# Optimization experiments

Measured on AMD Instinct MI355X. Metric: run time of the kernel, lower is better.

Reference implementation:

```python
import jax, jax.numpy as jnp
import numpy as np

B, N, HID = 4, 1024, 256
NH, DH = 8, 32          # heads, head dim (HID = NH*DH)
BH = 64                 # bias MLP hidden


def setup_inputs() -> dict:
    key = jax.random.key(0)
    ks = jax.random.split(key, 12)
    s = lambda fan_in: 1.0 / np.sqrt(fan_in)
    return {
        "h": jax.random.normal(ks[0], (B, N, HID), jnp.float32),
        "coord": jax.random.uniform(ks[1], (B, N), jnp.float32),
        "mask": jnp.ones((B, N), jnp.int32),
        # qkv / proj linear params (stored [in, out])
        "Wqkv": jax.random.normal(ks[2], (HID, 3 * HID), jnp.float32) * s(HID),
        "bqkv": jnp.zeros((3 * HID,), jnp.float32),
        "Wproj": jax.random.normal(ks[3], (HID, HID), jnp.float32) * s(HID),
        "bproj": jnp.zeros((HID,), jnp.float32),
        # layernorm
        "gamma": jnp.ones((HID,), jnp.float32),
        "beta": jnp.zeros((HID,), jnp.float32),
        # relative-bias MLP: Linear(1->BH), SiLU, Linear(BH->BH), SiLU, Linear(BH->NH)
        "Wb1": jax.random.normal(ks[4], (1, BH), jnp.float32),
        "bb1": jnp.zeros((BH,), jnp.float32),
        "Wb2": jax.random.normal(ks[5], (BH, BH), jnp.float32) * s(BH),
        "bb2": jnp.zeros((BH,), jnp.float32),
        "Wb3": jax.random.normal(ks[6], (BH, NH), jnp.float32) * s(BH),
        "bb3": jnp.zeros((NH,), jnp.float32),
    }


def _layernorm(x, gamma, beta, eps=1e-5):
    mu = jnp.mean(x, axis=-1, keepdims=True)
    var = jnp.mean((x - mu) ** 2, axis=-1, keepdims=True)
    return (x - mu) * jax.lax.rsqrt(var + eps) * gamma + beta


def reference(h, coord, mask, Wqkv, bqkv, Wproj, bproj, gamma, beta,
              Wb1, bb1, Wb2, bb2, Wb3, bb3):
    x = _layernorm(h, gamma, beta)                      # [B,N,HID]
    qkv = x @ Wqkv + bqkv                               # [B,N,3*HID]
    q, k, v = jnp.split(qkv, 3, axis=-1)
    # [B,N,HID] -> [B,NH,N,DH]
    reshape = lambda t: t.reshape(B, N, NH, DH).transpose(0, 2, 1, 3)
    q, k, v = reshape(q), reshape(k), reshape(v)

    attn = jnp.einsum("bhqd,bhkd->bhqk", q, k) / np.sqrt(DH).astype(np.float32)

    # pairwise coordinate differences and learned bias
    dcoord = coord[:, None, :] - coord[:, :, None]      # [B,N,N]
    t = dcoord[..., None]                               # [B,N,N,1]
    t = jax.nn.silu(t @ Wb1 + bb1)                      # [B,N,N,BH]
    t = jax.nn.silu(t @ Wb2 + bb2)                      # [B,N,N,BH]
    bias = (t @ Wb3 + bb3)                              # [B,N,N,NH]
    attn = attn + bias.transpose(0, 3, 1, 2)            # [B,NH,N,N]

    neg_inf = jnp.array(-jnp.inf, attn.dtype)
    attn = jnp.where(mask[:, None, None, :] == 0, neg_inf, attn)
    w = jax.nn.softmax(attn, axis=-1)

    out = jnp.einsum("bhqk,bhkd->bhqd", w, v)           # [B,NH,N,DH]
    out = out.transpose(0, 2, 1, 3).reshape(B, N, HID)
    out = out @ Wproj + bproj
    return h + out
```

## Files before the change

### kernel.cpp

```cpp
#include <hip/hip_runtime.h>
#include <hip/hip_fp16.h>
#include <hip/hip_bf16.h>
#include <math.h>

#define BB   4
#define NN   1024
#define HIDD 256
#define NHD  8
#define DHD  32
#define BHD  64
#define TI2  2048
#define TBSX 3592
#define NSPL 2
#define LOG2E 1.4426950408889634f

typedef __attribute__((ext_vector_type(8))) short bf16x8;
typedef __attribute__((ext_vector_type(4))) short bf16x4;
typedef __attribute__((ext_vector_type(4))) float f32x4;

__device__ __forceinline__ unsigned short f2bf(float x) {
  union { __hip_bfloat16 h; unsigned short u; } c;
  c.h = __float2bfloat16(x);
  return c.u;
}
__device__ __forceinline__ float bf2f(unsigned short b) {
  union { unsigned u; float f; } c; c.u = ((unsigned)b) << 16;
  return c.f;
}

__device__ __forceinline__ void pv_mfma(f32x4& acc, bf16x4 a, bf16x4 b) {
#if __has_builtin(__builtin_amdgcn_mfma_f32_16x16x16bf16_1k)
  acc = __builtin_amdgcn_mfma_f32_16x16x16bf16_1k(a, b, acc, 0, 0, 0);
#else
  asm volatile("s_nop 1\n\t"
               "v_mfma_f32_16x16x16_bf16 %0, %1, %2, %0\n\t"
               "s_nop 7\n\t"
               "s_nop 3"
               : "+v"(acc) : "v"(a), "v"(b));
#endif
}

__global__ __launch_bounds__(256) void prep_kernel(
    const float* __restrict__ Wb1, const float* __restrict__ bb1,
    const float* __restrict__ Wb2, const float* __restrict__ bb2,
    const float* __restrict__ Wb3, const float* __restrict__ bb3,
    const float* __restrict__ Wqkv, const float* __restrict__ Wproj,
    unsigned short* __restrict__ tblb, unsigned short* __restrict__ wtq,
    unsigned short* __restrict__ wtp)
{
  __shared__ float h1a[4][64], h2a[4][64];
  __shared__ float t[16][17];
  int bid = blockIdx.x, tid = threadIdx.x;
  if (bid < 513) {
    int g = tid >> 6, j = tid & 63;
    int pt = bid * 4 + g;
    float tt = -1.0f + (float)pt * (2.0f / (float)TI2);
    float z0 = fmaf(tt, Wb1[j], bb1[j]);
    h1a[g][j] = z0 / (1.0f + __expf(-z0));
    __syncthreads();
    float a0 = bb2[j];
    #pragma unroll 16
    for (int i = 0; i < BHD; ++i) a0 = fmaf(h1a[g][i], Wb2[i*BHD + j], a0);
    h2a[g][j] = a0 / (1.0f + __expf(-a0));
    __syncthreads();
    if (j < NHD && pt <= TI2) {
      float o0 = bb3[j];
      #pragma unroll 16
      for (int i = 0; i < BHD; ++i) o0 = fmaf(h2a[g][i], Wb3[i*NHD + j], o0);
      tblb[j*TBSX + pt] = f2bf(o0 * LOG2E);
    }
  } else if (bid < 521) {
    int head = bid - 513;
    unsigned short neg = f2bf(-1e31f);
    for (int i = tid; i < TBSX - (TI2 + 1); i += 256)
      tblb[head*TBSX + TI2 + 1 + i] = neg;
  } else {
    const float* W; unsigned short* Wt; int n0, k0, ncols;
    if (bid < 1289) {
      int rb = bid - 521;
      n0 = (rb % 48) * 16; k0 = (rb / 48) * 16; ncols = 768;
      W = Wqkv; Wt = wtq;
    } else {
      int rc = bid - 1289;
      n0 = (rc & 15) * 16; k0 = (rc >> 4) * 16; ncols = 256;
      W = Wproj; Wt = wtp;
    }
    int sx = tid & 15, sy = tid >> 4;
    t[sy][sx] = W[(size_t)(k0 + sy) * ncols + n0 + sx];
    __syncthreads();
    Wt[(size_t)(n0 + sy) * 256 + k0 + sx] = f2bf(t[sx][sy]);
  }
}

__global__ __launch_bounds__(256) void ln_qkv_mm_kernel(
    const float* __restrict__ h, const float* __restrict__ gamma,
    const float* __restrict__ beta, const unsigned short* __restrict__ Wt,
    const float* __restrict__ bqkv,
    unsigned short* __restrict__ qws, unsigned short* __restrict__ kws,
    unsigned short* __restrict__ vtws)
{
  __shared__ unsigned short xs[16][260];
  int tid = threadIdx.x;
  int m0 = blockIdx.x * 16, n0 = blockIdx.y * 128;

  {
    int r = tid >> 4, q = tid & 15;
    const float* hrow = h + (size_t)(m0 + r)*HIDD + q*16;
    float4 xv[4];
    float sum = 0.f, sq = 0.f;
    #pragma unroll
    for (int j = 0; j < 4; ++j) {
      xv[j] = *(const float4*)&hrow[j*4];
      sum += xv[j].x + xv[j].y + xv[j].z + xv[j].w;
      sq  += xv[j].x*xv[j].x + xv[j].y*xv[j].y + xv[j].z*xv[j].z + xv[j].w*xv[j].w;
    }
    sum += __shfl_xor(sum, 1); sq += __shfl_xor(sq, 1);
    sum += __shfl_xor(sum, 2); sq += __shfl_xor(sq, 2);
    sum += __shfl_xor(sum, 4); sq += __shfl_xor(sq, 4);
    sum += __shfl_xor(sum, 8); sq += __shfl_xor(sq, 8);
    float mu  = sum * (1.0f/HIDD);
    float var = sq  * (1.0f/HIDD) - mu*mu;
    float rs  = rsqrtf(var + 1e-5f);
    #pragma unroll
    for (int j2 = 0; j2 < 2; ++j2) {
      union { bf16x8 v; unsigned short u[8]; } o;
      #pragma unroll
      for (int e = 0; e < 2; ++e) {
        float4 x4 = xv[j2*2 + e];
        int col = q*16 + j2*8 + e*4;
        float4 gv = *(const float4*)&gamma[col];
        float4 bv = *(const float4*)&beta[col];
        o.u[e*4+0] = f2bf(fmaf((x4.x - mu)*rs, gv.x, bv.x));
        o.u[e*4+1] = f2bf(fmaf((x4.y - mu)*rs, gv.y, bv.y));
        o.u[e*4+2] = f2bf(fmaf((x4.z - mu)*rs, gv.z, bv.z));
        o.u[e*4+3] = f2bf(fmaf((x4.w - mu)*rs, gv.w, bv.w));
      }
      *(bf16x8*)&xs[r][q*16 + j2*8] = o.v;
    }
  }
  __syncthreads();

  int lane = tid & 63, w = tid >> 6;
  int lo = lane & 15, hi = lane >> 4;
  int cw = w * 32;
  f32x4 acc[2];
  acc[0] = (f32x4){0.f,0.f,0.f,0.f};
  acc[1] = (f32x4){0.f,0.f,0.f,0.f};

  #pragma unroll
  for (int ks = 0; ks < 8; ++ks) {
    bf16x8 af = *(const bf16x8*)&xs[lo][ks*32 + hi*8];
    #pragma unroll
    for (int nt = 0; nt < 2; ++nt) {
      bf16x8 bf = *(const bf16x8*)&Wt[(size_t)(n0 + cw + nt*16 + lo)*256 + ks*32 + hi*8];
      acc[nt] = __builtin_amdgcn_mfma_f32_16x16x32_bf16(af, bf, acc[nt], 0, 0, 0);
    }
  }

  int b = m0 >> 10;
  if (n0 < 512) {
    unsigned short* dst = (n0 < 256) ? qws : kws;
    int nbase = (m0 & 1023) + hi*4;
    #pragma unroll
    for (int nt = 0; nt < 2; ++nt) {
      int c = n0 + cw + nt*16 + lo;
      int cr = c & 255;
      int head = cr >> 5, d = cr & 31;
      float bq = bqkv[c];
      size_t bh = (size_t)(b*NHD + head);
      #pragma unroll
      for (int r = 0; r < 4; ++r)
        dst[(bh*NN + nbase + r)*DHD + d] = f2bf(acc[nt][r] + bq);
    }
  } else {
    __syncthreads();
    unsigned short (*vt)[20] = (unsigned short(*)[20])&xs[0][0];
    #pragma unroll
    for (int nt = 0; nt < 2; ++nt) {
      int cr = cw + nt*16 + lo;
      float bq = bqkv[n0 + cr];
      union { unsigned short u[4]; unsigned wd[2]; } pk;
      #pragma unroll
      for (int r = 0; r < 4; ++r) pk.u[r] = f2bf(acc[nt][r] + bq);
      int col = hi*4;
      *(unsigned*)&vt[cr][col]     = pk.wd[0];
      *(unsigned*)&vt[cr][col + 2] = pk.wd[1];
    }
    __syncthreads();
    int nn0 = m0 & 1023;
    int row = tid >> 1, ch = tid & 1;
    int cr256 = (n0 - 512) + row;
    int head = cr256 >> 5, d = cr256 & 31;
    *(bf16x8*)&vtws[((size_t)(b*NHD + head)*DHD + d)*NN + nn0 + ch*8] =
        *(const bf16x8*)&vt[row][ch*8];
  }
}

__global__ __launch_bounds__(256, 4) void attn_kernel(
    const unsigned short* __restrict__ Q, const unsigned short* __restrict__ K,
    const unsigned short* __restrict__ Vt, const float* __restrict__ coord,
    const int* __restrict__ mask, const unsigned short* __restrict__ tblb,
    unsigned short* __restrict__ pO, float* __restrict__ pL)
{
  __shared__ unsigned short tableL[TBSX];
  __shared__ unsigned short Klds[2][64][40];
  __shared__ unsigned short Vtlds[2][32][72];
  __shared__ __align__(16) float ckL[NN/NSPL];

  int tid = threadIdx.x, lane = tid & 63, w = tid >> 6;
  int bh = blockIdx.y, half = blockIdx.z;
  int b = bh >> 3, head = bh & 7;
  int qbase = blockIdx.x * 64 + w * 16;
  int lo = lane & 15, hi = lane >> 4;

  {
    const uint4* src = (const uint4*)(tblb + head*TBSX);
    uint4* dst = (uint4*)tableL;
    for (int i = tid; i < TBSX/8; i += 256) dst[i] = src[i];
  }

  bf16x8 qf = *(const bf16x8*)&Q[((size_t)bh*NN + qbase + lo)*DHD + hi*8];
  float qoff2 = fmaf(coord[b*NN + qbase + lo], -(float)TI2*0.5f, (float)TI2*0.5f);

  float l = 0.f;
  f32x4 oacc[2];
  oacc[0] = (f32x4){0.f,0.f,0.f,0.f};
  oacc[1] = (f32x4){0.f,0.f,0.f,0.f};
  const float scale2 = 0.17677669529663689f * LOG2E;

  int kt0 = half * (NN/NSPL);
  int sr = tid >> 2, ss = tid & 3;
  int vr = tid >> 3, vs = tid & 7;
  {
    #pragma unroll
    for (int i = 0; i < (NN/NSPL)/256; ++i) {
      int idx = i*256 + tid;
      ckL[idx] = mask[b*NN + kt0 + idx] ? coord[b*NN + kt0 + idx] : 2.5f;
    }
    *(bf16x8*)&Klds[0][sr][ss*8] =
        *(const bf16x8*)&K[((size_t)bh*NN + kt0 + sr)*DHD + ss*8];
    *(bf16x8*)&Vtlds[0][vr][vs*8] =
        *(const bf16x8*)&Vt[((size_t)bh*DHD + vr)*NN + kt0 + vs*8];
  }
  __syncthreads();

  for (int t = 0; t < NN/NSPL/64; ++t) {
    int kt = kt0 + t*64;
    int cur = t & 1;
    bf16x8 kn, vn;
    if (t < NN/NSPL/64 - 1) {
      kn = *(const bf16x8*)&K[((size_t)bh*NN + kt + 64 + sr)*DHD + ss*8];
      vn = *(const bf16x8*)&Vt[((size_t)bh*DHD + vr)*NN + kt + 64 + vs*8];
    }
    float ck[4][4];
    #pragma unroll
    for (int nt = 0; nt < 4; ++nt) {
      float4 c4 = *(const float4*)&ckL[t*64 + nt*16 + hi*4];
      ck[nt][0] = c4.x; ck[nt][1] = c4.y; ck[nt][2] = c4.z; ck[nt][3] = c4.w;
    }

    f32x4 z = {0.f,0.f,0.f,0.f};
    f32x4 sacc[4];
    #pragma unroll
    for (int nt = 0; nt < 4; ++nt) {
      bf16x8 kf = *(const bf16x8*)&Klds[cur][nt*16 + lo][hi*8];
      sacc[nt] = __builtin_amdgcn_mfma_f32_16x16x32_bf16(kf, qf, z, 0, 0, 0);
    }

    bf16x4 pfrag[4];
    #pragma unroll
    for (int nt = 0; nt < 4; ++nt) {
      float p[4];
      #pragma unroll
      for (int r = 0; r < 4; ++r) {
        float u = fmaf(ck[nt][r], (float)TI2*0.5f, qoff2);
        int i0 = (int)(u + 0.5f);
        float s = fmaf(sacc[nt][r], scale2, bf2f(tableL[i0]));
        p[r] = __builtin_amdgcn_exp2f(s);
      }
      l += (p[0] + p[1]) + (p[2] + p[3]);
      union { bf16x4 v; unsigned short u[4]; } pk;
      pk.u[0] = f2bf(p[0]); pk.u[1] = f2bf(p[1]);
      pk.u[2] = f2bf(p[2]); pk.u[3] = f2bf(p[3]);
      pfrag[nt] = pk.v;
    }

    #pragma unroll
    for (int nt = 0; nt < 4; ++nt) {
      #pragma unroll
      for (int n2 = 0; n2 < 2; ++n2) {
        bf16x4 vf = *(const bf16x4*)&Vtlds[cur][n2*16 + lo][nt*16 + hi*4];
        pv_mfma(oacc[n2], vf, pfrag[nt]);
      }
    }

    if (t < NN/NSPL/64 - 1) {
      *(bf16x8*)&Klds[cur^1][sr][ss*8] = kn;
      *(bf16x8*)&Vtlds[cur^1][vr][vs*8] = vn;
    }
    __syncthreads();
  }

  l += __shfl_xor(l, 16);
  l += __shfl_xor(l, 32);
  size_t base = ((size_t)(half*BB*NHD + bh)*NN + qbase + lo);
  #pragma unroll
  for (int n2 = 0; n2 < 2; ++n2) {
    union { bf16x4 v; unsigned short u[4]; } ov;
    ov.u[0] = f2bf(oacc[n2][0]); ov.u[1] = f2bf(oacc[n2][1]);
    ov.u[2] = f2bf(oacc[n2][2]); ov.u[3] = f2bf(oacc[n2][3]);
    *(bf16x4*)&pO[base*DHD + n2*16 + hi*4] = ov.v;
  }
  if (hi == 0) pL[base] = l;
}

__global__ __launch_bounds__(256) void proj_mm_kernel(
    const unsigned short* __restrict__ pO, const float* __restrict__ pL,
    const unsigned short* __restrict__ Wpt, const float* __restrict__ bp,
    const float* __restrict__ h, float* __restrict__ out)
{
  __shared__ unsigned short alds[32][264];
  int tid = threadIdx.x;
  int m0 = blockIdx.x * 32, n0 = blockIdx.y * 32;

  {
    int r = tid >> 3, q = tid & 7;
    int g = m0 + r, b = g >> 10, n = g & 1023;
    int bhh = b*NHD + q;
    float l0 = pL[(size_t)bhh*NN + n];
    float l1 = pL[(size_t)(BB*NHD)*NN + (size_t)bhh*NN + n];
    float inv = 1.0f / (l0 + l1);
    const bf16x8* p0 = (const bf16x8*)&pO[((size_t)bhh*NN + n)*DHD];
    const bf16x8* p1 = (const bf16x8*)&pO[(((size_t)(BB*NHD) + bhh)*NN + n)*DHD];
    #pragma unroll
    for (int j = 0; j < 4; ++j) {
      union { bf16x8 v; unsigned short u[8]; } a, c, o;
      a.v = p0[j]; c.v = p1[j];
      #pragma unroll
      for (int e = 0; e < 8; ++e)
        o.u[e] = f2bf((bf2f(a.u[e]) + bf2f(c.u[e])) * inv);
      *(bf16x8*)&alds[r][q*32 + j*8] = o.v;
    }
  }
  __syncthreads();

  int lane = tid & 63, w = tid >> 6;
  int lo = lane & 15, hi = lane >> 4;
  int mw = (w & 1) * 16;
  int nw = n0 + (w >> 1) * 16;
  f32x4 acc = (f32x4){0.f,0.f,0.f,0.f};

  #pragma unroll
  for (int ks = 0; ks < 8; ++ks) {
    bf16x8 af = *(const bf16x8*)&alds[mw + lo][ks*32 + hi*8];
    bf16x8 bf = *(const bf16x8*)&Wpt[(size_t)(nw + lo)*256 + ks*32 + hi*8];
    acc = __builtin_amdgcn_mfma_f32_16x16x32_bf16(af, bf, acc, 0, 0, 0);
  }

  int c = nw + lo;
  float bpv = bp[c];
  #pragma unroll
  for (int r = 0; r < 4; ++r) {
    size_t o = (size_t)(m0 + mw + hi*4 + r)*HIDD + c;
    out[o] = h[o] + acc[r] + bpv;
  }
}

extern "C" void kernel_launch(void* const* d_in, const int* in_sizes, int n_in,
                              void* d_out, int out_size, void* d_ws, size_t ws_size,
                              hipStream_t stream)
{
  const float* h     = (const float*)d_in[0];
  const float* coord = (const float*)d_in[1];
  const int*   mask  = (const int*)  d_in[2];
  const float* Wqkv  = (const float*)d_in[3];
  const float* bqkv  = (const float*)d_in[4];
  const float* Wproj = (const float*)d_in[5];
  const float* bproj = (const float*)d_in[6];
  const float* gamma = (const float*)d_in[7];
  const float* beta  = (const float*)d_in[8];
  const float* Wb1   = (const float*)d_in[9];
  const float* bb1   = (const float*)d_in[10];
  const float* Wb2   = (const float*)d_in[11];
  const float* bb2   = (const float*)d_in[12];
  const float* Wb3   = (const float*)d_in[13];
  const float* bb3   = (const float*)d_in[14];
  float* out = (float*)d_out;

  unsigned short* tblb = (unsigned short*)d_ws;
  float* pL = (float*)(tblb + NHD*TBSX);
  unsigned short* wtq  = (unsigned short*)(pL + (size_t)NSPL*BB*NHD*NN);
  unsigned short* wtp  = wtq + 768*256;
  unsigned short* qws  = wtp + 256*256;
  unsigned short* kws  = qws + (size_t)BB*NHD*NN*DHD;
  unsigned short* vtws = kws + (size_t)BB*NHD*NN*DHD;
  unsigned short* pO   = vtws + (size_t)BB*NHD*NN*DHD;

  prep_kernel<<<dim3(1545), dim3(256), 0, stream>>>(
      Wb1, bb1, Wb2, bb2, Wb3, bb3, Wqkv, Wproj, tblb, wtq, wtp);
  ln_qkv_mm_kernel<<<dim3(BB*NN/16, 6), dim3(256), 0, stream>>>(
      h, gamma, beta, wtq, bqkv, qws, kws, vtws);
  attn_kernel<<<dim3(NN/64, BB*NHD, NSPL), dim3(256), 0, stream>>>(
      qws, kws, vtws, coord, mask, tblb, pO, pL);
  proj_mm_kernel<<<dim3(BB*NN/32, HIDD/32), dim3(256), 0, stream>>>(
      pO, pL, wtp, bproj, h, out);
}
```

Measured before the change: 59.38 us.

## Move bias-table MLP into QKV kernel, prescale coords, add MFMA priority hints

Moves the relative-bias lookup-table MLP out of the prep kernel and into an extra grid row of the LN+QKV kernel. That shortens the prep kernel's critical path and lets the table computation overlap with the QKV GEMM blocks. In the attention inner loop, key coordinates are pre-multiplied by the table scale and the rounding offset is folded into the query offset, which removes an FMA and an add per score element. Raises wave priority around the MFMA blocks with s_setprio. The table is now built by a kernel that also does heavier GEMM work, which may change load balance.

```diff
diff --git a/kernel.cpp b/kernel.cpp
--- a/kernel.cpp
+++ b/kernel.cpp
@@ -41,68 +41,73 @@
 }
 
 __global__ __launch_bounds__(256) void prep_kernel(
-    const float* __restrict__ Wb1, const float* __restrict__ bb1,
-    const float* __restrict__ Wb2, const float* __restrict__ bb2,
-    const float* __restrict__ Wb3, const float* __restrict__ bb3,
     const float* __restrict__ Wqkv, const float* __restrict__ Wproj,
-    unsigned short* __restrict__ tblb, unsigned short* __restrict__ wtq,
-    unsigned short* __restrict__ wtp)
+    unsigned short* __restrict__ wtq, unsigned short* __restrict__ wtp)
 {
-  __shared__ float h1a[4][64], h2a[4][64];
   __shared__ float t[16][17];
   int bid = blockIdx.x, tid = threadIdx.x;
-  if (bid < 513) {
-    int g = tid >> 6, j = tid & 63;
-    int pt = bid * 4 + g;
-    float tt = -1.0f + (float)pt * (2.0f / (float)TI2);
-    float z0 = fmaf(tt, Wb1[j], bb1[j]);
-    h1a[g][j] = z0 / (1.0f + __expf(-z0));
-    __syncthreads();
-    float a0 = bb2[j];
-    #pragma unroll 16
-    for (int i = 0; i < BHD; ++i) a0 = fmaf(h1a[g][i], Wb2[i*BHD + j], a0);
-    h2a[g][j] = a0 / (1.0f + __expf(-a0));
-    __syncthreads();
-    if (j < NHD && pt <= TI2) {
-      float o0 = bb3[j];
-      #pragma unroll 16
-      for (int i = 0; i < BHD; ++i) o0 = fmaf(h2a[g][i], Wb3[i*NHD + j], o0);
-      tblb[j*TBSX + pt] = f2bf(o0 * LOG2E);
-    }
-  } else if (bid < 521) {
-    int head = bid - 513;
-    unsigned short neg = f2bf(-1e31f);
-    for (int i = tid; i < TBSX - (TI2 + 1); i += 256)
-      tblb[head*TBSX + TI2 + 1 + i] = neg;
+  const float* W; unsigned short* Wt; int n0, k0, ncols;
+  if (bid < 768) {
+    n0 = (bid % 48) * 16; k0 = (bid / 48) * 16; ncols = 768;
+    W = Wqkv; Wt = wtq;
   } else {
-    const float* W; unsigned short* Wt; int n0, k0, ncols;
-    if (bid < 1289) {
-      int rb = bid - 521;
-      n0 = (rb % 48) * 16; k0 = (rb / 48) * 16; ncols = 768;
-      W = Wqkv; Wt = wtq;
-    } else {
-      int rc = bid - 1289;
-      n0 = (rc & 15) * 16; k0 = (rc >> 4) * 16; ncols = 256;
-      W = Wproj; Wt = wtp;
-    }
-    int sx = tid & 15, sy = tid >> 4;
-    t[sy][sx] = W[(size_t)(k0 + sy) * ncols + n0 + sx];
-    __syncthreads();
-    Wt[(size_t)(n0 + sy) * 256 + k0 + sx] = f2bf(t[sx][sy]);
-  }
+    int rc = bid - 768;
+    n0 = (rc & 15) * 16; k0 = (rc >> 4) * 16; ncols = 256;
+    W = Wproj; Wt = wtp;
+  }
+  int sx = tid & 15, sy = tid >> 4;
+  t[sy][sx] = W[(size_t)(k0 + sy) * ncols + n0 + sx];
+  __syncthreads();
+  Wt[(size_t)(n0 + sy) * 256 + k0 + sx] = f2bf(t[sx][sy]);
 }
 
 __global__ __launch_bounds__(256) void ln_qkv_mm_kernel(
     const float* __restrict__ h, const float* __restrict__ gamma,
     const float* __restrict__ beta, const unsigned short* __restrict__ Wt,
     const float* __restrict__ bqkv,
+    const float* __restrict__ Wb1, const float* __restrict__ bb1,
+    const float* __restrict__ Wb2, const float* __restrict__ bb2,
+    const float* __restrict__ Wb3, const float* __restrict__ bb3,
+    unsigned short* __restrict__ tblb,
     unsigned short* __restrict__ qws, unsigned short* __restrict__ kws,
     unsigned short* __restrict__ vtws)
 {
   __shared__ unsigned short xs[16][260];
+  __shared__ float th1[4][64], th2[4][64];
   int tid = threadIdx.x;
+
+  if (blockIdx.y == 6) {
+    int x = blockIdx.x;
+    int g = tid >> 6, j = tid & 63;
+    int npass = (x == 0) ? 3 : 2;
+    for (int ps = 0; ps < npass; ++ps) {
+      int pt = (ps < 2) ? (x*8 + ps*4 + g) : TI2;
+      float tt = -1.0f + (float)pt * (2.0f / (float)TI2);
+      float z0 = fmaf(tt, Wb1[j], bb1[j]);
+      th1[g][j] = z0 / (1.0f + __expf(-z0));
+      __syncthreads();
+      float a0 = bb2[j];
+      #pragma unroll 16
+      for (int i = 0; i < BHD; ++i) a0 = fmaf(th1[g][i], Wb2[i*BHD + j], a0);
+      th2[g][j] = a0 / (1.0f + __expf(-a0));
+      __syncthreads();
+      if (j < NHD) {
+        float o0 = bb3[j];
+        #pragma unroll 16
+        for (int i = 0; i < BHD; ++i) o0 = fmaf(th2[g][i], Wb3[i*NHD + j], o0);
+        tblb[j*TBSX + pt] = f2bf(o0 * LOG2E);
+      }
+      __syncthreads();
+    }
+    if (x < NHD) {
+      unsigned short neg = f2bf(-1e31f);
+      for (int i = tid; i < TBSX - (TI2 + 1); i += 256)
+        tblb[x*TBSX + TI2 + 1 + i] = neg;
+    }
+    return;
+  }
+
   int m0 = blockIdx.x * 16, n0 = blockIdx.y * 128;
-
   {
     int r = tid >> 4, q = tid & 15;
     const float* hrow = h + (size_t)(m0 + r)*HIDD + q*16;
@@ -220,7 +225,8 @@
   }
 
   bf16x8 qf = *(const bf16x8*)&Q[((size_t)bh*NN + qbase + lo)*DHD + hi*8];
-  float qoff2 = fmaf(coord[b*NN + qbase + lo], -(float)TI2*0.5f, (float)TI2*0.5f);
+  float qoff2 = fmaf(coord[b*NN + qbase + lo], -(float)TI2*0.5f,
+                     (float)TI2*0.5f + 0.5f);
 
   float l = 0.f;
   f32x4 oacc[2];
@@ -235,7 +241,8 @@
     #pragma unroll
     for (int i = 0; i < (NN/NSPL)/256; ++i) {
       int idx = i*256 + tid;
-      ckL[idx] = mask[b*NN + kt0 + idx] ? coord[b*NN + kt0 + idx] : 2.5f;
+      ckL[idx] = (mask[b*NN + kt0 + idx] ? coord[b*NN + kt0 + idx] : 2.5f)
+                 * ((float)TI2*0.5f);
     }
     *(bf16x8*)&Klds[0][sr][ss*8] =
         *(const bf16x8*)&K[((size_t)bh*NN + kt0 + sr)*DHD + ss*8];
@@ -261,11 +268,13 @@
 
     f32x4 z = {0.f,0.f,0.f,0.f};
     f32x4 sacc[4];
+    __builtin_amdgcn_s_setprio(1);
     #pragma unroll
     for (int nt = 0; nt < 4; ++nt) {
       bf16x8 kf = *(const bf16x8*)&Klds[cur][nt*16 + lo][hi*8];
       sacc[nt] = __builtin_amdgcn_mfma_f32_16x16x32_bf16(kf, qf, z, 0, 0, 0);
     }
+    __builtin_amdgcn_s_setprio(0);
 
     bf16x4 pfrag[4];
     #pragma unroll
@@ -273,8 +282,7 @@
       float p[4];
       #pragma unroll
       for (int r = 0; r < 4; ++r) {
-        float u = fmaf(ck[nt][r], (float)TI2*0.5f, qoff2);
-        int i0 = (int)(u + 0.5f);
+        int i0 = (int)(ck[nt][r] + qoff2);
         float s = fmaf(sacc[nt][r], scale2, bf2f(tableL[i0]));
         p[r] = __builtin_amdgcn_exp2f(s);
       }
@@ -285,6 +293,7 @@
       pfrag[nt] = pk.v;
     }
 
+    __builtin_amdgcn_s_setprio(1);
     #pragma unroll
     for (int nt = 0; nt < 4; ++nt) {
       #pragma unroll
@@ -293,6 +302,7 @@
         pv_mfma(oacc[n2], vf, pfrag[nt]);
       }
     }
+    __builtin_amdgcn_s_setprio(0);
 
     if (t < NN/NSPL/64 - 1) {
       *(bf16x8*)&Klds[cur^1][sr][ss*8] = kn;
@@ -396,10 +406,10 @@
   unsigned short* vtws = kws + (size_t)BB*NHD*NN*DHD;
   unsigned short* pO   = vtws + (size_t)BB*NHD*NN*DHD;
 
-  prep_kernel<<<dim3(1545), dim3(256), 0, stream>>>(
-      Wb1, bb1, Wb2, bb2, Wb3, bb3, Wqkv, Wproj, tblb, wtq, wtp);
-  ln_qkv_mm_kernel<<<dim3(BB*NN/16, 6), dim3(256), 0, stream>>>(
-      h, gamma, beta, wtq, bqkv, qws, kws, vtws);
+  prep_kernel<<<dim3(1024), dim3(256), 0, stream>>>(Wqkv, Wproj, wtq, wtp);
+  ln_qkv_mm_kernel<<<dim3(BB*NN/16, 7), dim3(256), 0, stream>>>(
+      h, gamma, beta, wtq, bqkv, Wb1, bb1, Wb2, bb2, Wb3, bb3, tblb,
+      qws, kws, vtws);
   attn_kernel<<<dim3(NN/64, BB*NHD, NSPL), dim3(256), 0, stream>>>(
       qws, kws, vtws, coord, mask, tblb, pO, pL);
   proj_mm_kernel<<<dim3(BB*NN/32, HIDD/32), dim3(256), 0, stream>>>(
```

New measurement: 62.58 us. 1.05x slower.
